# Optimization experiments

Measured on AMD Instinct MI355X. Metric: run time of the kernel, lower is better.

Reference implementation:

```python
import jax, jax.numpy as jnp
import numpy as np

FEATURE_DIM = 6272
UNITS = 32
B, L = 8, 256

def setup_inputs() -> dict:
    key = jax.random.key(0)
    k1, k2, k3, k4, k5 = jax.random.split(key, 5)
    return {
        "inputs": jax.random.normal(k1, (B, L, FEATURE_DIM), dtype=jnp.float32),
        "Wt": jax.random.normal(k2, (FEATURE_DIM, UNITS), dtype=jnp.float32) * 0.02,
        "bh": jax.random.normal(k3, (UNITS,), dtype=jnp.float32),
        "Wa": jax.random.normal(k4, (UNITS, 1), dtype=jnp.float32) * 0.02,
        "ba": jax.random.normal(k5, (1,), dtype=jnp.float32),
    }

def reference(inputs, Wt, bh, Wa, ba):
    # q == k: both projected through Wt (original code reuses Wt for both)
    p = jnp.einsum('blf,fu->blu', inputs, Wt)            # [B, L, U]
    # additive (Bahdanau-style) pairwise combine: [B, L, L, U]
    beta = jnp.tanh(p[:, :, None, :] + p[:, None, :, :] + bh)
    alpha = jnp.einsum('bqku,uo->bqk', beta, Wa) + ba[0]  # [B, L, L]
    alpha = jax.nn.sigmoid(alpha)
    a = jax.nn.softmax(alpha, axis=-1)                    # softmax over keys
    c_r = jnp.einsum('bqk,bkf->bqf', a, inputs)           # [B, L, F]
    return c_r
```

## Files before the change

### kernel.cpp

```cpp
#include <hip/hip_runtime.h>
#include <hip/hip_bf16.h>
#include <math.h>

#define FDIM 6272
#define LQ   256
#define BN   8
#define UDIM 32
#define BL   (BN*LQ)
#define WTS  904

typedef short  short8 __attribute__((ext_vector_type(8)));
typedef float  f32x4  __attribute__((ext_vector_type(4)));

static __device__ __forceinline__ ushort f2bf(float f) {
    __hip_bfloat16 h = __float2bfloat16(f);
    return *(ushort*)&h;
}
static __device__ __forceinline__ float fexp2(float x) {
    float r;
    asm volatile("v_exp_f32 %0, %1 \n s_nop 1" : "=v"(r) : "v"(x));
    return r;
}
static __device__ __forceinline__ float frcp(float x) {
    float r;
    asm volatile("v_rcp_f32 %0, %1 \n s_nop 1" : "=v"(r) : "v"(x));
    return r;
}
static __device__ __forceinline__ float tanh_fast(float v) {
    return 1.f - 2.f * frcp(1.f + fexp2(v * 2.88539008177793f));
}

__global__ __launch_bounds__(256)
void k1_mfma(const float* __restrict__ x, const float* __restrict__ Wt,
             float* __restrict__ pbp, ushort* __restrict__ xb16) {
    __shared__ ushort wtt_s[UDIM * WTS];

    const int t  = threadIdx.x;
    const int f0 = blockIdx.y * 896;

    {
        const int fl0 = t >> 3;
        const int u4  = (t & 7) * 4;
        #pragma unroll
        for (int s = 0; s < 28; ++s) {
            const int fl = s * 32 + fl0;
            const float4 w4 = *(const float4*)(Wt + (size_t)(f0 + fl) * UDIM + u4);
            wtt_s[(u4 + 0) * WTS + fl] = f2bf(w4.x);
            wtt_s[(u4 + 1) * WTS + fl] = f2bf(w4.y);
            wtt_s[(u4 + 2) * WTS + fl] = f2bf(w4.z);
            wtt_s[(u4 + 3) * WTS + fl] = f2bf(w4.w);
        }
    }
    __syncthreads();

    const int wv   = t >> 6, lane = t & 63;
    const int n16  = lane & 15, quad = lane >> 4;
    const int row0 = blockIdx.x * 32 + 16 * (wv & 1);
    const int u0   = 16 * (wv >> 1);

    const float*  xr = x + (size_t)(row0 + n16) * FDIM + f0 + quad * 8;
    const ushort* wr = wtt_s + (u0 + n16) * WTS + quad * 8;
    ushort*       xw = xb16 + (size_t)(row0 + n16) * FDIM + f0 + quad * 8;

    f32x4 acc = (f32x4){0.f, 0.f, 0.f, 0.f};

    #pragma unroll 4
    for (int c = 0; c < 28; ++c) {
        const float4 a0 = *(const float4*)(xr + c * 32);
        const float4 a1 = *(const float4*)(xr + c * 32 + 4);
        short8 af;
        af[0] = (short)f2bf(a0.x); af[1] = (short)f2bf(a0.y);
        af[2] = (short)f2bf(a0.z); af[3] = (short)f2bf(a0.w);
        af[4] = (short)f2bf(a1.x); af[5] = (short)f2bf(a1.y);
        af[6] = (short)f2bf(a1.z); af[7] = (short)f2bf(a1.w);
        if (wv < 2)
            *(short8*)(xw + c * 32) = af;
        const short8 bf = *(const short8*)(wr + c * 32);
        acc = __builtin_amdgcn_mfma_f32_16x16x32_bf16(af, bf, acc, 0, 0, 0);
    }

    float* pb = pbp + (size_t)blockIdx.y * BL * UDIM;
    #pragma unroll
    for (int r = 0; r < 4; ++r)
        pb[(size_t)(row0 + quad * 4 + r) * UDIM + u0 + n16] = acc[r];
}

__global__ __launch_bounds__(256)
void k2_attn(const float* __restrict__ pbp, const float* __restrict__ bh,
             const float* __restrict__ Wa, const float* __restrict__ ba,
             ushort* __restrict__ ab) {
    const int blk = blockIdx.x;
    const int b   = blk >> 6, qt = blk & 63;
    const int k   = threadIdx.x;

    __shared__ float pk_s[LQ * 33];
    __shared__ float pq_s[4][UDIM];
    __shared__ float wa_s[UDIM];
    __shared__ float red[4][4];

    if (k < UDIM) wa_s[k] = Wa[k];
    const float* pbb = pbp + (size_t)b * LQ * UDIM;
    #pragma unroll
    for (int i = 0; i < 8; ++i) {
        const int e = 4 * k + 1024 * i;
        float4 v = *(const float4*)(pbb + e);
        #pragma unroll
        for (int y = 1; y < 7; ++y) {
            const float4 p = *(const float4*)(pbb + (size_t)y * BL * UDIM + e);
            v.x += p.x; v.y += p.y; v.z += p.z; v.w += p.w;
        }
        float* d = &pk_s[(e >> 5) * 33 + (e & 31)];
        d[0] = v.x; d[1] = v.y; d[2] = v.z; d[3] = v.w;
    }
    __syncthreads();
    if (k < 4 * UDIM) {
        const int j = k >> 5, u = k & 31;
        pq_s[j][u] = pk_s[(qt * 4 + j) * 33 + u] + bh[u];
    }
    __syncthreads();

    const float* pk = &pk_s[k * 33];
    float pkr[UDIM];
    #pragma unroll
    for (int u = 0; u < UDIM; ++u) pkr[u] = pk[u];

    const float ba0 = ba[0];
    float e4[4];
    #pragma unroll
    for (int j = 0; j < 4; ++j) {
        float s = 0.f;
        #pragma unroll
        for (int u = 0; u < UDIM; ++u)
            s = fmaf(tanh_fast(pq_s[j][u] + pkr[u]), wa_s[u], s);

        const float alpha = frcp(1.f + fexp2(-(s + ba0) * 1.44269504088896f));
        const float e = fexp2(alpha * 1.44269504088896f);
        e4[j] = e;

        float v = e;
        #pragma unroll
        for (int m = 1; m < 64; m <<= 1) v += __shfl_xor(v, m, 64);
        if ((k & 63) == 0) red[j][k >> 6] = v;
    }
    __syncthreads();
    #pragma unroll
    for (int j = 0; j < 4; ++j) {
        const float tot = red[j][0] + red[j][1] + red[j][2] + red[j][3];
        ab[((size_t)b * LQ + qt * 4 + j) * LQ + k] = f2bf(e4[j] * frcp(tot));
    }
}

__global__ __launch_bounds__(256)
void k3_fused(const ushort* __restrict__ xb16, const ushort* __restrict__ ab,
              float* __restrict__ out) {
    __shared__ ushort Bs[2][64 * 72];

    const int t    = threadIdx.x;
    const int f0   = blockIdx.x * 64;
    const int b    = blockIdx.y;
    const int wv   = t >> 6;
    const int lane = t & 63;
    const int n16  = lane & 15;
    const int quad = lane >> 4;
    const int g    = t >> 4;
    const int kp   = t & 15;

    const ushort* xb  = xb16 + (size_t)b * LQ * FDIM + f0 + 4 * g;
    const ushort* abb = ab   + (size_t)b * LQ * LQ;

    f32x4 acc[4][4];
    #pragma unroll
    for (int mf = 0; mf < 4; ++mf)
        #pragma unroll
        for (int nf = 0; nf < 4; ++nf)
            acc[mf][nf] = (f32x4){0.f, 0.f, 0.f, 0.f};

    uint2 r0, r1, r2, r3;
#define LDX(kc) do {                                                      \
        r0 = *(const uint2*)(xb + (size_t)((kc) + 2 * kp     ) * FDIM);   \
        r1 = *(const uint2*)(xb + (size_t)((kc) + 2 * kp +  1) * FDIM);   \
        r2 = *(const uint2*)(xb + (size_t)((kc) + 2 * kp + 32) * FDIM);   \
        r3 = *(const uint2*)(xb + (size_t)((kc) + 2 * kp + 33) * FDIM);   \
    } while (0)
#define STX(bufi) do {                                                    \
        unsigned* bw = (unsigned*)(Bs[bufi]);                             \
        bw[(4 * g + 0) * 36 + kp]      = (r0.x & 0xffffu) | (r1.x << 16); \
        bw[(4 * g + 1) * 36 + kp]      = (r0.x >> 16) | (r1.x & 0xffff0000u); \
        bw[(4 * g + 2) * 36 + kp]      = (r0.y & 0xffffu) | (r1.y << 16); \
        bw[(4 * g + 3) * 36 + kp]      = (r0.y >> 16) | (r1.y & 0xffff0000u); \
        bw[(4 * g + 0) * 36 + kp + 16] = (r2.x & 0xffffu) | (r3.x << 16); \
        bw[(4 * g + 1) * 36 + kp + 16] = (r2.x >> 16) | (r3.x & 0xffff0000u); \
        bw[(4 * g + 2) * 36 + kp + 16] = (r2.y & 0xffffu) | (r3.y << 16); \
        bw[(4 * g + 3) * 36 + kp + 16] = (r2.y >> 16) | (r3.y & 0xffff0000u); \
    } while (0)

    LDX(0);
    STX(0);

    for (int c = 0; c < 4; ++c) {
        if (c < 3) LDX((c + 1) * 64);
        short8 af[4][2];
        #pragma unroll
        for (int mf = 0; mf < 4; ++mf)
            #pragma unroll
            for (int h = 0; h < 2; ++h)
                af[mf][h] = *(const short8*)(abb
                    + (size_t)(64 * wv + 16 * mf + n16) * LQ
                    + c * 64 + h * 32 + quad * 8);
        __syncthreads();
        const ushort* bsc = Bs[c & 1];
        #pragma unroll
        for (int h = 0; h < 2; ++h)
            #pragma unroll
            for (int nf = 0; nf < 4; ++nf) {
                const short8 bf = *(const short8*)(bsc + (16 * nf + n16) * 72
                                                   + h * 32 + quad * 8);
                #pragma unroll
                for (int mf = 0; mf < 4; ++mf)
                    acc[mf][nf] = __builtin_amdgcn_mfma_f32_16x16x32_bf16(
                        af[mf][h], bf, acc[mf][nf], 0, 0, 0);
            }
        if (c < 3) STX((c + 1) & 1);
    }
#undef LDX
#undef STX

    float* ob = out + ((size_t)b * LQ + 64 * wv + quad * 4) * FDIM + f0 + n16;
    #pragma unroll
    for (int mf = 0; mf < 4; ++mf)
        #pragma unroll
        for (int nf = 0; nf < 4; ++nf)
            #pragma unroll
            for (int r = 0; r < 4; ++r)
                ob[(size_t)(16 * mf + r) * FDIM + 16 * nf] = acc[mf][nf][r];
}

extern "C" void kernel_launch(void* const* d_in, const int* in_sizes, int n_in,
                              void* d_out, int out_size, void* d_ws, size_t ws_size,
                              hipStream_t stream) {
    const float* x  = (const float*)d_in[0];
    const float* Wt = (const float*)d_in[1];
    const float* bh = (const float*)d_in[2];
    const float* Wa = (const float*)d_in[3];
    const float* ba = (const float*)d_in[4];
    float* out = (float*)d_out;

    float*  pbp  = (float*)d_ws;
    ushort* ab   = (ushort*)((char*)d_ws + 2097152);
    ushort* xb16 = (ushort*)((char*)d_ws + 2097152 + 1048576);

    k1_mfma<<<dim3(64, 7), 256, 0, stream>>>(x, Wt, pbp, xb16);
    k2_attn<<<512, 256, 0, stream>>>(pbp, bh, Wa, ba, ab);
    k3_fused<<<dim3(98, 8), 256, 0, stream>>>(xb16, ab, out);
}
```

Before: 161.2 us.

## Retile projection kernel so each wave covers both unit halves with finer F split

The projection kernel now gives each wave 16 rows and both 16-unit halves, two MFMAs per A fragment. Each input element is therefore loaded and converted to bf16 once instead of twice across waves, and all waves write the bf16 copy. The F dimension is split into 14 chunks of 448 instead of 7 chunks of 896, keeping the grid at 448 blocks and halving the shared-memory footprint. In exchange the attention kernel must reduce 14 partial projections instead of 7, and the partial buffer doubles, which shifts the workspace offsets.

New measurement: 156.7 us. -2.8%, faster.

```diff
diff --git a/kernel.cpp b/kernel.cpp
--- a/kernel.cpp
+++ b/kernel.cpp
@@ -7,7 +7,9 @@
 #define BN   8
 #define UDIM 32
 #define BL   (BN*LQ)
-#define WTS  904
+#define FSPL 448
+#define NSPL 14
+#define WTS2 456
 
 typedef short  short8 __attribute__((ext_vector_type(8)));
 typedef float  f32x4  __attribute__((ext_vector_type(4)));
@@ -33,39 +35,40 @@
 __global__ __launch_bounds__(256)
 void k1_mfma(const float* __restrict__ x, const float* __restrict__ Wt,
              float* __restrict__ pbp, ushort* __restrict__ xb16) {
-    __shared__ ushort wtt_s[UDIM * WTS];
+    __shared__ ushort wtt_s[UDIM * WTS2];
 
     const int t  = threadIdx.x;
-    const int f0 = blockIdx.y * 896;
+    const int f0 = blockIdx.y * FSPL;
 
     {
         const int fl0 = t >> 3;
         const int u4  = (t & 7) * 4;
         #pragma unroll
-        for (int s = 0; s < 28; ++s) {
+        for (int s = 0; s < NSPL; ++s) {
             const int fl = s * 32 + fl0;
             const float4 w4 = *(const float4*)(Wt + (size_t)(f0 + fl) * UDIM + u4);
-            wtt_s[(u4 + 0) * WTS + fl] = f2bf(w4.x);
-            wtt_s[(u4 + 1) * WTS + fl] = f2bf(w4.y);
-            wtt_s[(u4 + 2) * WTS + fl] = f2bf(w4.z);
-            wtt_s[(u4 + 3) * WTS + fl] = f2bf(w4.w);
+            wtt_s[(u4 + 0) * WTS2 + fl] = f2bf(w4.x);
+            wtt_s[(u4 + 1) * WTS2 + fl] = f2bf(w4.y);
+            wtt_s[(u4 + 2) * WTS2 + fl] = f2bf(w4.z);
+            wtt_s[(u4 + 3) * WTS2 + fl] = f2bf(w4.w);
         }
     }
     __syncthreads();
 
     const int wv   = t >> 6, lane = t & 63;
     const int n16  = lane & 15, quad = lane >> 4;
-    const int row0 = blockIdx.x * 32 + 16 * (wv & 1);
-    const int u0   = 16 * (wv >> 1);
-
-    const float*  xr = x + (size_t)(row0 + n16) * FDIM + f0 + quad * 8;
-    const ushort* wr = wtt_s + (u0 + n16) * WTS + quad * 8;
-    ushort*       xw = xb16 + (size_t)(row0 + n16) * FDIM + f0 + quad * 8;
-
-    f32x4 acc = (f32x4){0.f, 0.f, 0.f, 0.f};
-
-    #pragma unroll 4
-    for (int c = 0; c < 28; ++c) {
+    const int row0 = blockIdx.x * 64 + 16 * wv;
+
+    const float*  xr  = x + (size_t)(row0 + n16) * FDIM + f0 + quad * 8;
+    const ushort* wr0 = wtt_s + (     n16) * WTS2 + quad * 8;
+    const ushort* wr1 = wtt_s + (16 + n16) * WTS2 + quad * 8;
+    ushort*       xw  = xb16 + (size_t)(row0 + n16) * FDIM + f0 + quad * 8;
+
+    f32x4 acc0 = (f32x4){0.f, 0.f, 0.f, 0.f};
+    f32x4 acc1 = (f32x4){0.f, 0.f, 0.f, 0.f};
+
+    #pragma unroll 7
+    for (int c = 0; c < NSPL; ++c) {
         const float4 a0 = *(const float4*)(xr + c * 32);
         const float4 a1 = *(const float4*)(xr + c * 32 + 4);
         short8 af;
@@ -73,16 +76,19 @@
         af[2] = (short)f2bf(a0.z); af[3] = (short)f2bf(a0.w);
         af[4] = (short)f2bf(a1.x); af[5] = (short)f2bf(a1.y);
         af[6] = (short)f2bf(a1.z); af[7] = (short)f2bf(a1.w);
-        if (wv < 2)
-            *(short8*)(xw + c * 32) = af;
-        const short8 bf = *(const short8*)(wr + c * 32);
-        acc = __builtin_amdgcn_mfma_f32_16x16x32_bf16(af, bf, acc, 0, 0, 0);
+        *(short8*)(xw + c * 32) = af;
+        const short8 b0 = *(const short8*)(wr0 + c * 32);
+        const short8 b1 = *(const short8*)(wr1 + c * 32);
+        acc0 = __builtin_amdgcn_mfma_f32_16x16x32_bf16(af, b0, acc0, 0, 0, 0);
+        acc1 = __builtin_amdgcn_mfma_f32_16x16x32_bf16(af, b1, acc1, 0, 0, 0);
     }
 
     float* pb = pbp + (size_t)blockIdx.y * BL * UDIM;
     #pragma unroll
-    for (int r = 0; r < 4; ++r)
-        pb[(size_t)(row0 + quad * 4 + r) * UDIM + u0 + n16] = acc[r];
+    for (int r = 0; r < 4; ++r) {
+        pb[(size_t)(row0 + quad * 4 + r) * UDIM +      n16] = acc0[r];
+        pb[(size_t)(row0 + quad * 4 + r) * UDIM + 16 + n16] = acc1[r];
+    }
 }
 
 __global__ __launch_bounds__(256)
@@ -105,7 +111,7 @@
         const int e = 4 * k + 1024 * i;
         float4 v = *(const float4*)(pbb + e);
         #pragma unroll
-        for (int y = 1; y < 7; ++y) {
+        for (int y = 1; y < NSPL; ++y) {
             const float4 p = *(const float4*)(pbb + (size_t)y * BL * UDIM + e);
             v.x += p.x; v.y += p.y; v.z += p.z; v.w += p.w;
         }
@@ -246,10 +252,10 @@
     float* out = (float*)d_out;
 
     float*  pbp  = (float*)d_ws;
-    ushort* ab   = (ushort*)((char*)d_ws + 2097152);
-    ushort* xb16 = (ushort*)((char*)d_ws + 2097152 + 1048576);
-
-    k1_mfma<<<dim3(64, 7), 256, 0, stream>>>(x, Wt, pbp, xb16);
+    ushort* ab   = (ushort*)((char*)d_ws + 4194304);
+    ushort* xb16 = (ushort*)((char*)d_ws + 4194304 + 1048576);
+
+    k1_mfma<<<dim3(32, NSPL), 256, 0, stream>>>(x, Wt, pbp, xb16);
     k2_attn<<<512, 256, 0, stream>>>(pbp, bh, Wa, ba, ab);
     k3_fused<<<dim3(98, 8), 256, 0, stream>>>(xb16, ab, out);
 }
```
